# Kernel optimization log

Measured on AMD Instinct MI355X. Metric: run time of the kernel, lower is better.

## Reference

```python
import jax, jax.numpy as jnp
import numpy as np

H = 256   # hidden_dim
NH = 8    # attention heads, embed_dim = 2*H

def _ln(x, g, b, eps=1e-5):
    m = x.mean(-1, keepdims=True)
    v = ((x - m) ** 2).mean(-1, keepdims=True)
    return (x - m) / jnp.sqrt(v + eps) * g + b


def setup_inputs() -> dict:
    key = jax.random.key(0)
    ks = jax.random.split(key, 16)
    B, T, R, P = 32, 2048, 16, 2
    E = 2 * H
    s = 0.02
    n = lambda k, shp: (jax.random.normal(k, shp, jnp.float32) * s)
    z = lambda shp: jnp.zeros(shp, jnp.float32)
    return {
        "encoded_tasks": jax.random.normal(ks[0], (B, T, E), jnp.float32),
        "context": jax.random.normal(ks[1], (B, H), jnp.float32),
        "preference": jax.random.uniform(ks[2], (B, P), dtype=jnp.float32),
        "pref_W": n(ks[3], (P, H)), "pref_b": z((H,)),
        "ln_g": jnp.ones((H,), jnp.float32), "ln_b": z((H,)),
        "Wq": n(ks[4], (E, E)), "bq": z((E,)),
        "Wk": n(ks[5], (E, E)), "bk": z((E,)),
        "Wv": n(ks[6], (E, E)), "bv": z((E,)),
        "Wo": n(ks[7], (E, E)), "bo": z((E,)),
        "W_ih": n(ks[8], (4 * H, 3 * H)), "b_ih": z((4 * H,)),
        "W_hh": n(ks[9], (4 * H, H)), "b_hh": z((4 * H,)),
        "hW1": n(ks[10], (3 * H, H)), "hb1": z((H,)),
        "hW2": n(ks[11], (H, R)), "hb2": z((R,)),
        "num_steps": 32,
    }


def reference(encoded_tasks, context, preference, pref_W, pref_b, ln_g, ln_b,
              Wq, bq, Wk, bk, Wv, bv, Wo, bo,
              W_ih, b_ih, W_hh, b_hh, hW1, hb1, hW2, hb2, num_steps):
    B, T, E = encoded_tasks.shape
    Dh = E // NH
    scale = 1.0 / jnp.sqrt(jnp.float32(Dh))
    # preference encoder: Linear -> ReLU -> LayerNorm
    pref = _ln(jax.nn.relu(preference @ pref_W + pref_b), ln_g, ln_b)  # [B, H]
    # K/V projections of encoded_tasks are step-invariant: compute once
    K = (encoded_tasks @ Wk + bk).reshape(B, T, NH, Dh)
    V = (encoded_tasks @ Wv + bv).reshape(B, T, NH, Dh)
    h0 = context[:, :H]
    c0 = jnp.zeros_like(h0)

    def step(carry, _):
        h, c = carry
        q = jnp.concatenate([h, pref], axis=-1)              # [B, 2H]
        qh = (q @ Wq + bq).reshape(B, NH, Dh) * scale
        scores = jnp.einsum('bhd,bthd->bht', qh, K)
        w = jax.nn.softmax(scores, axis=-1)
        attn = jnp.einsum('bht,bthd->bhd', w, V).reshape(B, E)
        ctx = attn @ Wo + bo                                  # [B, 2H]
        x = jnp.concatenate([h, ctx[:, :H], pref], axis=-1)   # [B, 3H]
        gates = x @ W_ih.T + b_ih + h @ W_hh.T + b_hh         # [B, 4H]
        i, f, g, o = jnp.split(gates, 4, axis=-1)
        c_new = jax.nn.sigmoid(f) * c + jax.nn.sigmoid(i) * jnp.tanh(g)
        h_new = jax.nn.sigmoid(o) * jnp.tanh(c_new)
        dec = jnp.concatenate([h_new, ctx[:, :H], pref], axis=-1)
        logits = jax.nn.relu(dec @ hW1 + hb1) @ hW2 + hb2     # [B, R]
        return (h_new, c_new), logits

    (_, _), logits = jax.lax.scan(step, (h0, c0), None, length=num_steps)
    return jnp.transpose(logits, (1, 0, 2))  # [B, num_steps, R]
```

## Files before the change

kernel.cpp:

```cpp
#include <hip/hip_runtime.h>
#include <hip/hip_bf16.h>


typedef __bf16 bf16;
typedef __attribute__((ext_vector_type(8))) __bf16 bf16x8;
typedef __attribute__((ext_vector_type(4))) __bf16 bf16x4;
typedef __attribute__((ext_vector_type(4))) float f32x4;
typedef __attribute__((ext_vector_type(2))) float f32x2;

#define B_  32
#define T_  2048
#define H_  256
#define S_  32

static __device__ __forceinline__ float sigmoidf_(float x){ return 1.f/(1.f+__expf(-x)); }
static __device__ __forceinline__ float tanhf_(float x){ float e=__expf(2.f*x); return (e-1.f)/(e+1.f); }

__global__ void prep_misc(const float* __restrict__ Wq, const float* __restrict__ Wk,
                          const float* __restrict__ Wv, const float* __restrict__ Wo,
                          const float* __restrict__ Wih, const float* __restrict__ Whh,
                          const float* __restrict__ context,
                          bf16* __restrict__ WkvT, bf16* __restrict__ WqT, bf16* __restrict__ WoT,
                          bf16* __restrict__ WihB, bf16* __restrict__ WhhB,
                          float* __restrict__ h0, float* __restrict__ c0, float* __restrict__ ctxz)
{
  const int total = 524288+262144+131072+786432+262144+8192+8192+262144;
  for (int i = blockIdx.x*blockDim.x + threadIdx.x; i < total; i += gridDim.x*blockDim.x){
    int x = i;
    if (x < 524288){ int n = x>>9, k = x&511;
      WkvT[x] = (bf16)(n<512 ? Wk[k*512+n] : Wv[k*512+(n-512)]); continue; }
    x -= 524288;
    if (x < 262144){ int n = x>>9, k = x&511; WqT[x] = (bf16)Wq[k*512+n]; continue; }
    x -= 262144;
    if (x < 131072){ int h = x>>14, rem = x&16383, j = rem>>6, d = rem&63;
      WoT[x] = (bf16)Wo[(h*64+d)*512 + j]; continue; }
    x -= 131072;
    if (x < 786432){ WihB[x] = (bf16)Wih[x]; continue; }
    x -= 786432;
    if (x < 262144){ WhhB[x] = (bf16)Whh[x]; continue; }
    x -= 262144;
    if (x < 8192){ h0[x] = context[x]; continue; }
    x -= 8192;
    if (x < 8192){ c0[x] = 0.f; continue; }
    x -= 8192;
    ctxz[x] = 0.f;
  }
}

__global__ __launch_bounds__(256) void prep_pref(const float* __restrict__ preference,
                                                 const float* __restrict__ pref_W,
                                                 const float* __restrict__ pref_b,
                                                 const float* __restrict__ ln_g,
                                                 const float* __restrict__ ln_b,
                                                 float* __restrict__ prefb)
{
  __shared__ float red_[4];
  int b = blockIdx.x, j = threadIdx.x;
  float p0 = preference[b*2], p1 = preference[b*2+1];
  float v = fmaxf(p0*pref_W[j] + p1*pref_W[256+j] + pref_b[j], 0.f);
  float s = v;
  #pragma unroll
  for (int o=32;o;o>>=1) s += __shfl_xor(s,o);
  if ((j&63)==0) red_[j>>6] = s;
  __syncthreads();
  float mean = (red_[0]+red_[1]+red_[2]+red_[3]) * (1.f/256.f);
  __syncthreads();
  float d = v - mean;
  float s2 = d*d;
  #pragma unroll
  for (int o=32;o;o>>=1) s2 += __shfl_xor(s2,o);
  if ((j&63)==0) red_[j>>6] = s2;
  __syncthreads();
  float var = (red_[0]+red_[1]+red_[2]+red_[3]) * (1.f/256.f);
  prefb[b*256+j] = d * rsqrtf(var + 1e-5f) * ln_g[j] + ln_b[j];
}

__global__ __launch_bounds__(256) void gemm_kv(const float* __restrict__ X,
                                               const bf16* __restrict__ WkvT,
                                               const float* __restrict__ bk, const float* __restrict__ bv,
                                               unsigned char* __restrict__ Kf8, unsigned char* __restrict__ Vf8)
{
  __shared__ __align__(16) bf16 As[128*40];
  __shared__ __align__(16) bf16 Bs[128*40];
  int blk = blockIdx.x;
  int bm = ((blk>>6)<<3) | (blk&7);
  int bn = (blk>>3)&7;
  int m0 = bm<<7, n0 = bn<<7;
  int tid = threadIdx.x;
  int lane = tid&63, wave = tid>>6;
  int wm = (wave>>1)<<6, wn = (wave&1)<<6;
  int q = lane>>4, li = lane&15;
  int r = tid>>1, half = tid&1;
  const float* Xrow = &X[(size_t)(m0+r)*512 + half*16];
  const bf16*  Brow = &WkvT[(size_t)(n0+r)*512 + half*16];
  f32x4 acc[4][4];
  #pragma unroll
  for (int a=0;a<4;a++)
    #pragma unroll
    for (int b=0;b<4;b++) acc[a][b] = (f32x4){0.f,0.f,0.f,0.f};

  float4 apf[4]; bf16x8 bpf[2];
  #pragma unroll
  for (int i=0;i<4;i++) apf[i] = *(const float4*)(Xrow + i*4);
  bpf[0] = *(const bf16x8*)(Brow);
  bpf[1] = *(const bf16x8*)(Brow + 8);

  for (int k0=0;k0<512;k0+=32){
    __syncthreads();
    #pragma unroll
    for (int i=0;i<4;i++){
      bf16x4 a4; a4[0]=(bf16)apf[i].x; a4[1]=(bf16)apf[i].y; a4[2]=(bf16)apf[i].z; a4[3]=(bf16)apf[i].w;
      *(bf16x4*)&As[r*40 + half*16 + i*4] = a4;
    }
    *(bf16x8*)&Bs[r*40 + half*16]     = bpf[0];
    *(bf16x8*)&Bs[r*40 + half*16 + 8] = bpf[1];
    __syncthreads();
    if (k0+32 < 512){
      #pragma unroll
      for (int i=0;i<4;i++) apf[i] = *(const float4*)(Xrow + k0+32 + i*4);
      bpf[0] = *(const bf16x8*)(Brow + k0+32);
      bpf[1] = *(const bf16x8*)(Brow + k0+40);
    }
    bf16x8 af[4], bfr[4];
    #pragma unroll
    for (int mt=0;mt<4;mt++) af[mt] = *(const bf16x8*)&As[(wm+mt*16+li)*40 + q*8];
    #pragma unroll
    for (int nt=0;nt<4;nt++) bfr[nt] = *(const bf16x8*)&Bs[(wn+nt*16+li)*40 + q*8];
    #pragma unroll
    for (int mt=0;mt<4;mt++)
      #pragma unroll
      for (int nt=0;nt<4;nt++)
        acc[mt][nt] = __builtin_amdgcn_mfma_f32_16x16x32_bf16(bfr[nt], af[mt], acc[mt][nt], 0,0,0);
  }
  #pragma unroll
  for (int mt=0;mt<4;mt++){
    int mm = m0 + wm + mt*16 + li;
    int b = mm>>11, t = mm&2047;
    #pragma unroll
    for (int nt=0;nt<4;nt++){
      int nb = n0 + wn + nt*16 + q*4;
      const float* bias = (nb<512) ? (bk+nb) : (bv+nb-512);
      unsigned char* dst = (nb<512) ? Kf8 : Vf8;
      int nn = nb & 511;
      int h = nn>>6, d0 = nn&63;
      unsigned int p = 0;
      p = __builtin_amdgcn_cvt_pk_fp8_f32(acc[mt][nt][0]+bias[0], acc[mt][nt][1]+bias[1], p, false);
      p = __builtin_amdgcn_cvt_pk_fp8_f32(acc[mt][nt][2]+bias[2], acc[mt][nt][3]+bias[3], p, true);
      *(unsigned int*)&dst[(((size_t)(b*8+h))*T_ + (size_t)t)*64 + d0] = p;
    }
  }
}

__global__ __launch_bounds__(1024) void attn_step(const unsigned char* __restrict__ Kf8,
                                                  const unsigned char* __restrict__ Vf8,
                                                  const bf16* __restrict__ WqT, const bf16* __restrict__ WoT,
                                                  const float* __restrict__ bq, const float* __restrict__ prefb,
                                                  const float* __restrict__ h_prev, float* __restrict__ ctx_s)
{
  __shared__ float q_s[512];
  __shared__ float qh_s[64];
  __shared__ float aw[16][64];
  __shared__ float zw[16];
  __shared__ float attn_s[64];
  int b = blockIdx.x>>3, h = blockIdx.x&7;
  int tid = threadIdx.x;
  if (tid < 512) q_s[tid] = (tid<256) ? h_prev[b*256+tid] : prefb[b*256+(tid-256)];
  __syncthreads();
  {
    int d = tid>>4, p = tid&15;
    const bf16* wr = &WqT[(size_t)(h*64+d)*512 + p*32];
    const float* qq = &q_s[p*32];
    float s = 0.f;
    #pragma unroll
    for (int i=0;i<4;i++){
      bf16x8 w8 = *(const bf16x8*)&wr[i*8];
      #pragma unroll
      for (int j=0;j<8;j++) s += qq[i*8+j]*(float)w8[j];
    }
    s += __shfl_xor(s,1); s += __shfl_xor(s,2); s += __shfl_xor(s,4); s += __shfl_xor(s,8);
    if (p==0) qh_s[d] = (s + bq[h*64+d])*0.125f;
  }
  __syncthreads();
  int lane = tid&63, wave = tid>>6;
  int ro = lane>>2, dq = lane&3;
  float qhf[16];
  #pragma unroll
  for (int j=0;j<16;j++) qhf[j] = qh_s[dq*16+j];
  const unsigned char* Kb = Kf8 + ((size_t)(b*8+h))*T_*64;
  const unsigned char* Vb = Vf8 + ((size_t)(b*8+h))*T_*64;
  float acc[16];
  #pragma unroll
  for (int j=0;j<16;j++) acc[j]=0.f;
  float z = 0.f;
  #pragma unroll
  for (int it=0; it<8; ++it){
    int t = it*256 + wave*16 + ro;
    uint4 k4 = *(const uint4*)&Kb[(size_t)t*64 + dq*16];
    uint4 v4 = *(const uint4*)&Vb[(size_t)t*64 + dq*16];
    float s = 0.f;
    { f32x2 t0, t1;
      t0 = __builtin_amdgcn_cvt_pk_f32_fp8(k4.x,false); t1 = __builtin_amdgcn_cvt_pk_f32_fp8(k4.x,true);
      s += qhf[0]*t0.x + qhf[1]*t0.y + qhf[2]*t1.x + qhf[3]*t1.y;
      t0 = __builtin_amdgcn_cvt_pk_f32_fp8(k4.y,false); t1 = __builtin_amdgcn_cvt_pk_f32_fp8(k4.y,true);
      s += qhf[4]*t0.x + qhf[5]*t0.y + qhf[6]*t1.x + qhf[7]*t1.y;
      t0 = __builtin_amdgcn_cvt_pk_f32_fp8(k4.z,false); t1 = __builtin_amdgcn_cvt_pk_f32_fp8(k4.z,true);
      s += qhf[8]*t0.x + qhf[9]*t0.y + qhf[10]*t1.x + qhf[11]*t1.y;
      t0 = __builtin_amdgcn_cvt_pk_f32_fp8(k4.w,false); t1 = __builtin_amdgcn_cvt_pk_f32_fp8(k4.w,true);
      s += qhf[12]*t0.x + qhf[13]*t0.y + qhf[14]*t1.x + qhf[15]*t1.y;
    }
    s += __shfl_xor(s,1); s += __shfl_xor(s,2);
    float e = __expf(fminf(s, 80.f));
    z += e;
    { f32x2 t0, t1;
      t0 = __builtin_amdgcn_cvt_pk_f32_fp8(v4.x,false); t1 = __builtin_amdgcn_cvt_pk_f32_fp8(v4.x,true);
      acc[0]+=e*t0.x; acc[1]+=e*t0.y; acc[2]+=e*t1.x; acc[3]+=e*t1.y;
      t0 = __builtin_amdgcn_cvt_pk_f32_fp8(v4.y,false); t1 = __builtin_amdgcn_cvt_pk_f32_fp8(v4.y,true);
      acc[4]+=e*t0.x; acc[5]+=e*t0.y; acc[6]+=e*t1.x; acc[7]+=e*t1.y;
      t0 = __builtin_amdgcn_cvt_pk_f32_fp8(v4.z,false); t1 = __builtin_amdgcn_cvt_pk_f32_fp8(v4.z,true);
      acc[8]+=e*t0.x; acc[9]+=e*t0.y; acc[10]+=e*t1.x; acc[11]+=e*t1.y;
      t0 = __builtin_amdgcn_cvt_pk_f32_fp8(v4.w,false); t1 = __builtin_amdgcn_cvt_pk_f32_fp8(v4.w,true);
      acc[12]+=e*t0.x; acc[13]+=e*t0.y; acc[14]+=e*t1.x; acc[15]+=e*t1.y;
    }
  }
  #pragma unroll
  for (int j=0;j<16;j++){
    acc[j] += __shfl_xor(acc[j],4);
    acc[j] += __shfl_xor(acc[j],8);
    acc[j] += __shfl_xor(acc[j],16);
    acc[j] += __shfl_xor(acc[j],32);
  }
  z += __shfl_xor(z,4); z += __shfl_xor(z,8); z += __shfl_xor(z,16); z += __shfl_xor(z,32);
  if (ro==0){
    #pragma unroll
    for (int j=0;j<16;j++) aw[wave][dq*16+j] = acc[j];
    if (dq==0) zw[wave] = z;
  }
  __syncthreads();
  if (tid < 64){
    float Z = 0.f, a = 0.f;
    #pragma unroll
    for (int w=0;w<16;w++){ Z += zw[w]; a += aw[w][tid]; }
    attn_s[tid] = a / Z;
  }
  __syncthreads();
  {
    int j = tid>>2, p4 = tid&3;
    const bf16* wo = &WoT[(((size_t)h*256)+j)*64 + p4*16];
    const float* at = &attn_s[p4*16];
    float cp = 0.f;
    #pragma unroll
    for (int i=0;i<2;i++){
      bf16x8 w8 = *(const bf16x8*)&wo[i*8];
      #pragma unroll
      for (int u=0;u<8;u++) cp += at[i*8+u]*(float)w8[u];
    }
    cp += __shfl_xor(cp,1); cp += __shfl_xor(cp,2);
    if (p4==0) atomicAdd(&ctx_s[b*256+j], cp);
  }
}

__global__ __launch_bounds__(256) void gates_lstm(const float* __restrict__ h_prev, const float* __restrict__ ctx_s,
                                                  const float* __restrict__ prefb, const float* __restrict__ bo,
                                                  const bf16* __restrict__ WihB, const bf16* __restrict__ WhhB,
                                                  const float* __restrict__ b_ih, const float* __restrict__ b_hh,
                                                  const float* __restrict__ c_prev,
                                                  float* __restrict__ c_out, float* __restrict__ h_out)
{
  __shared__ __align__(16) bf16 xs[32*1032];
  __shared__ float gsum[2][32][18];
  int bk = blockIdx.x;
  int tid = threadIdx.x;
  #pragma unroll
  for (int i=0;i<32;i++){
    int u = i*256 + tid;
    int bb = u>>8, kq = u&255;
    int k = kq*4;
    float v0,v1,v2,v3;
    if (k < 256){
      const float* p = &h_prev[bb*256+k];
      v0=p[0];v1=p[1];v2=p[2];v3=p[3];
    } else if (k < 512){
      int j2 = k-256;
      const float* p = &ctx_s[bb*256+j2];
      v0=p[0]+bo[j2]; v1=p[1]+bo[j2+1]; v2=p[2]+bo[j2+2]; v3=p[3]+bo[j2+3];
    } else if (k < 768){
      const float* p = &prefb[bb*256+(k-512)];
      v0=p[0];v1=p[1];v2=p[2];v3=p[3];
    } else {
      const float* p = &h_prev[bb*256+(k-768)];
      v0=p[0];v1=p[1];v2=p[2];v3=p[3];
    }
    bf16x4 w4; w4[0]=(bf16)v0; w4[1]=(bf16)v1; w4[2]=(bf16)v2; w4[3]=(bf16)v3;
    *(bf16x4*)&xs[bb*1032+k] = w4;
  }
  __syncthreads();
  int lane = tid&63, wave = tid>>6;
  int q = lane>>4, li = lane&15;
  int mt = wave&1, kh = wave>>1;
  int n = (li>>2)*256 + bk*4 + (li&3);
  f32x4 acc = (f32x4){0.f,0.f,0.f,0.f};
  #pragma unroll 4
  for (int kk = kh*512; kk < kh*512+512; kk += 32){
    bf16x8 af = *(const bf16x8*)&xs[(mt*16+li)*1032 + kk + q*8];
    int kg = kk + q*8;
    const bf16* wp = (kg<768) ? &WihB[(size_t)n*768 + kg] : &WhhB[(size_t)n*256 + (kg-768)];
    bf16x8 bfrag = *(const bf16x8*)wp;
    acc = __builtin_amdgcn_mfma_f32_16x16x32_bf16(af, bfrag, acc, 0,0,0);
  }
  #pragma unroll
  for (int r=0;r<4;r++) gsum[kh][mt*16 + q*4 + r][li] = acc[r];
  __syncthreads();
  if (tid < 128){
    int b2 = tid>>2, j2 = tid&3;
    float val[4];
    #pragma unroll
    for (int gg=0; gg<4; gg++){
      int ng = gg*256 + bk*4 + j2;
      val[gg] = gsum[0][b2][gg*4+j2] + gsum[1][b2][gg*4+j2] + b_ih[ng] + b_hh[ng];
    }
    int J = bk*4 + j2;
    float cp = c_prev[b2*256+J];
    float cn = sigmoidf_(val[1])*cp + sigmoidf_(val[0])*tanhf_(val[2]);
    float hn = sigmoidf_(val[3])*tanhf_(cn);
    c_out[b2*256+J] = cn;
    h_out[b2*256+J] = hn;
  }
}

__global__ __launch_bounds__(256) void epilogue_k(const float* __restrict__ h_hist, const float* __restrict__ ctx_all,
                                                  const float* __restrict__ bo,
                                                  const float* __restrict__ prefb, const float* __restrict__ hW1,
                                                  const float* __restrict__ hb1, const float* __restrict__ hW2,
                                                  const float* __restrict__ hb2, float* __restrict__ out)
{
  __shared__ float dec[8][768];
  __shared__ float hid[8][260];
  int blk = blockIdx.x;
  int tid = threadIdx.x;
  #pragma unroll
  for (int i=0;i<8;i++){
    int sb = blk*8+i;
    int s = sb>>5, b = sb&31;
    for (int k=tid; k<768; k+=256){
      float v;
      if (k<256)      v = h_hist[((size_t)(s+1)*32 + b)*256 + k];
      else if (k<512) v = ctx_all[((size_t)s*32 + b)*256 + (k-256)] + bo[k-256];
      else            v = prefb[b*256 + (k-512)];
      dec[i][k] = v;
    }
  }
  __syncthreads();
  float a[8];
  #pragma unroll
  for (int i=0;i<8;i++) a[i]=0.f;
  for (int k=0;k<768;k++){
    float w = hW1[(size_t)k*256 + tid];
    #pragma unroll
    for (int i=0;i<8;i++) a[i] += dec[i][k]*w;
  }
  float b1 = hb1[tid];
  #pragma unroll
  for (int i=0;i<8;i++) hid[i][tid] = fmaxf(a[i]+b1, 0.f);
  __syncthreads();
  if (tid < 128){
    int i = tid>>4, r = tid&15;
    float s2 = 0.f;
    for (int j2=0;j2<256;j2++) s2 += hid[i][j2]*hW2[j2*16+r];
    s2 += hb2[r];
    int sb = blk*8+i;
    int st = sb>>5, b = sb&31;
    out[(size_t)b*512 + st*16 + r] = s2;
  }
}

extern "C" void kernel_launch(void* const* d_in, const int* in_sizes, int n_in,
                              void* d_out, int out_size, void* d_ws, size_t ws_size,
                              hipStream_t stream)
{
  const float* X          = (const float*)d_in[0];
  const float* context    = (const float*)d_in[1];
  const float* preference = (const float*)d_in[2];
  const float* pref_W     = (const float*)d_in[3];
  const float* pref_b     = (const float*)d_in[4];
  const float* ln_g       = (const float*)d_in[5];
  const float* ln_b       = (const float*)d_in[6];
  const float* Wq         = (const float*)d_in[7];
  const float* bq         = (const float*)d_in[8];
  const float* Wk         = (const float*)d_in[9];
  const float* bk         = (const float*)d_in[10];
  const float* Wv         = (const float*)d_in[11];
  const float* bv         = (const float*)d_in[12];
  const float* Wo         = (const float*)d_in[13];
  const float* bo         = (const float*)d_in[14];
  const float* W_ih       = (const float*)d_in[15];
  const float* b_ih       = (const float*)d_in[16];
  const float* W_hh       = (const float*)d_in[17];
  const float* b_hh       = (const float*)d_in[18];
  const float* hW1        = (const float*)d_in[19];
  const float* hb1        = (const float*)d_in[20];
  const float* hW2        = (const float*)d_in[21];
  const float* hb2        = (const float*)d_in[22];
  float* out = (float*)d_out;

  char* ws = (char*)d_ws;
  size_t off = 0;
  auto alloc = [&](size_t bytes)->char*{ char* p = ws+off; off += (bytes+255)&~(size_t)255; return p; };
  unsigned char* Kf8 = (unsigned char*)alloc((size_t)B_*8*T_*64);
  unsigned char* Vf8 = (unsigned char*)alloc((size_t)B_*8*T_*64);
  bf16* WkvT    = (bf16*)alloc(1024ull*512*2);
  bf16* WqT     = (bf16*)alloc(512ull*512*2);
  bf16* WoT     = (bf16*)alloc(8ull*256*64*2);
  bf16* WihB    = (bf16*)alloc(1024ull*768*2);
  bf16* WhhB    = (bf16*)alloc(1024ull*256*2);
  float* prefb  = (float*)alloc(8192ull*4);
  float* h_hist = (float*)alloc(33ull*8192*4);
  float* c_hist = (float*)alloc(33ull*8192*4);
  float* ctx_all= (float*)alloc(32ull*8192*4);
  (void)ws_size; (void)in_sizes; (void)n_in; (void)out_size;

  hipLaunchKernelGGL(prep_misc, dim3(512), dim3(256), 0, stream,
                     Wq,Wk,Wv,Wo,W_ih,W_hh,context,
                     WkvT,WqT,WoT,WihB,WhhB, h_hist, c_hist, ctx_all);
  hipLaunchKernelGGL(prep_pref, dim3(32), dim3(256), 0, stream,
                     preference, pref_W, pref_b, ln_g, ln_b, prefb);
  hipLaunchKernelGGL(gemm_kv, dim3(4096), dim3(256), 0, stream, X, WkvT, bk, bv, Kf8, Vf8);
  for (int s=0;s<S_;s++){
    hipLaunchKernelGGL(attn_step, dim3(256), dim3(1024), 0, stream,
                       Kf8, Vf8, WqT, WoT, bq, prefb,
                       h_hist + (size_t)s*8192, ctx_all + (size_t)s*8192);
    hipLaunchKernelGGL(gates_lstm, dim3(64), dim3(256), 0, stream,
                       h_hist + (size_t)s*8192, ctx_all + (size_t)s*8192,
                       prefb, bo, WihB, WhhB, b_ih, b_hh,
                       c_hist + (size_t)s*8192,
                       c_hist + (size_t)(s+1)*8192, h_hist + (size_t)(s+1)*8192);
  }
  hipLaunchKernelGGL(epilogue_k, dim3(128), dim3(256), 0, stream,
                     h_hist, ctx_all, bo, prefb, hW1, hb1, hW2, hb2, out);
}
```

Measured before the change: 1.730 ms.

## Fuse recurrent steps into one cooperative persistent kernel with grid syncs

Replaces the 64 per-step launches of attention and LSTM-gate kernels with a single cooperative kernel that loops over steps and uses grid.sync between phases. Per-head context partials go to a buffer instead of atomics, and each block computes a slice of the LSTM gates in fp32 straight from the original weights. X is also pre-converted to bf16 in the prep kernel so the K/V GEMM loads bf16 directly. The aims are to remove launch overhead and to halve GEMM A-operand traffic. The cost is grid-wide barriers, fp32 gate weight reads every step, and an extra pass over X to convert it.

```diff
diff --git a/kernel.cpp b/kernel.cpp
--- a/kernel.cpp
+++ b/kernel.cpp
@@ -1,5 +1,8 @@
 #include <hip/hip_runtime.h>
 #include <hip/hip_bf16.h>
+#include <hip/hip_cooperative_groups.h>
+
+namespace cg = cooperative_groups;
 
 
 typedef __bf16 bf16;
@@ -16,17 +19,24 @@
 static __device__ __forceinline__ float sigmoidf_(float x){ return 1.f/(1.f+__expf(-x)); }
 static __device__ __forceinline__ float tanhf_(float x){ float e=__expf(2.f*x); return (e-1.f)/(e+1.f); }
 
-__global__ void prep_misc(const float* __restrict__ Wq, const float* __restrict__ Wk,
+#define NX4_ 8388608
+__global__ void prep_misc(const float* __restrict__ X,
+                          const float* __restrict__ Wq, const float* __restrict__ Wk,
                           const float* __restrict__ Wv, const float* __restrict__ Wo,
-                          const float* __restrict__ Wih, const float* __restrict__ Whh,
                           const float* __restrict__ context,
+                          bf16* __restrict__ Xb,
                           bf16* __restrict__ WkvT, bf16* __restrict__ WqT, bf16* __restrict__ WoT,
-                          bf16* __restrict__ WihB, bf16* __restrict__ WhhB,
-                          float* __restrict__ h0, float* __restrict__ c0, float* __restrict__ ctxz)
-{
-  const int total = 524288+262144+131072+786432+262144+8192+8192+262144;
+                          float* __restrict__ h0, float* __restrict__ c0)
+{
+  const int total = NX4_ + 524288+262144+131072+8192+8192;
   for (int i = blockIdx.x*blockDim.x + threadIdx.x; i < total; i += gridDim.x*blockDim.x){
-    int x = i;
+    if (i < NX4_){
+      float4 x4 = *(const float4*)&X[(size_t)i*4];
+      bf16x4 o; o[0]=(bf16)x4.x; o[1]=(bf16)x4.y; o[2]=(bf16)x4.z; o[3]=(bf16)x4.w;
+      *(bf16x4*)&Xb[(size_t)i*4] = o;
+      continue;
+    }
+    int x = i - NX4_;
     if (x < 524288){ int n = x>>9, k = x&511;
       WkvT[x] = (bf16)(n<512 ? Wk[k*512+n] : Wv[k*512+(n-512)]); continue; }
     x -= 524288;
@@ -35,15 +45,9 @@
     if (x < 131072){ int h = x>>14, rem = x&16383, j = rem>>6, d = rem&63;
       WoT[x] = (bf16)Wo[(h*64+d)*512 + j]; continue; }
     x -= 131072;
-    if (x < 786432){ WihB[x] = (bf16)Wih[x]; continue; }
-    x -= 786432;
-    if (x < 262144){ WhhB[x] = (bf16)Whh[x]; continue; }
-    x -= 262144;
     if (x < 8192){ h0[x] = context[x]; continue; }
     x -= 8192;
-    if (x < 8192){ c0[x] = 0.f; continue; }
-    x -= 8192;
-    ctxz[x] = 0.f;
+    c0[x] = 0.f;
   }
 }
 
@@ -75,7 +79,7 @@
   prefb[b*256+j] = d * rsqrtf(var + 1e-5f) * ln_g[j] + ln_b[j];
 }
 
-__global__ __launch_bounds__(256) void gemm_kv(const float* __restrict__ X,
+__global__ __launch_bounds__(256) void gemm_kv(const bf16* __restrict__ Xb,
                                                const bf16* __restrict__ WkvT,
                                                const float* __restrict__ bk, const float* __restrict__ bv,
                                                unsigned char* __restrict__ Kf8, unsigned char* __restrict__ Vf8)
@@ -90,36 +94,32 @@
   int lane = tid&63, wave = tid>>6;
   int wm = (wave>>1)<<6, wn = (wave&1)<<6;
   int q = lane>>4, li = lane&15;
-  int r = tid>>1, half = tid&1;
-  const float* Xrow = &X[(size_t)(m0+r)*512 + half*16];
-  const bf16*  Brow = &WkvT[(size_t)(n0+r)*512 + half*16];
+  int r0 = tid>>2, oct = tid&3;
+  const bf16* A0 = &Xb[(size_t)(m0+r0)*512 + oct*8];
+  const bf16* A1 = A0 + (size_t)64*512;
+  const bf16* B0 = &WkvT[(size_t)(n0+r0)*512 + oct*8];
+  const bf16* B1 = B0 + (size_t)64*512;
   f32x4 acc[4][4];
   #pragma unroll
   for (int a=0;a<4;a++)
     #pragma unroll
     for (int b=0;b<4;b++) acc[a][b] = (f32x4){0.f,0.f,0.f,0.f};
 
-  float4 apf[4]; bf16x8 bpf[2];
-  #pragma unroll
-  for (int i=0;i<4;i++) apf[i] = *(const float4*)(Xrow + i*4);
-  bpf[0] = *(const bf16x8*)(Brow);
-  bpf[1] = *(const bf16x8*)(Brow + 8);
+  bf16x8 apf0 = *(const bf16x8*)A0, apf1 = *(const bf16x8*)A1;
+  bf16x8 bpf0 = *(const bf16x8*)B0, bpf1 = *(const bf16x8*)B1;
 
   for (int k0=0;k0<512;k0+=32){
     __syncthreads();
-    #pragma unroll
-    for (int i=0;i<4;i++){
-      bf16x4 a4; a4[0]=(bf16)apf[i].x; a4[1]=(bf16)apf[i].y; a4[2]=(bf16)apf[i].z; a4[3]=(bf16)apf[i].w;
-      *(bf16x4*)&As[r*40 + half*16 + i*4] = a4;
-    }
-    *(bf16x8*)&Bs[r*40 + half*16]     = bpf[0];
-    *(bf16x8*)&Bs[r*40 + half*16 + 8] = bpf[1];
+    *(bf16x8*)&As[r0*40+oct*8]      = apf0;
+    *(bf16x8*)&As[(r0+64)*40+oct*8] = apf1;
+    *(bf16x8*)&Bs[r0*40+oct*8]      = bpf0;
+    *(bf16x8*)&Bs[(r0+64)*40+oct*8] = bpf1;
     __syncthreads();
     if (k0+32 < 512){
-      #pragma unroll
-      for (int i=0;i<4;i++) apf[i] = *(const float4*)(Xrow + k0+32 + i*4);
-      bpf[0] = *(const bf16x8*)(Brow + k0+32);
-      bpf[1] = *(const bf16x8*)(Brow + k0+40);
+      apf0 = *(const bf16x8*)(A0 + k0+32);
+      apf1 = *(const bf16x8*)(A1 + k0+32);
+      bpf0 = *(const bf16x8*)(B0 + k0+32);
+      bpf1 = *(const bf16x8*)(B1 + k0+32);
     }
     bf16x8 af[4], bfr[4];
     #pragma unroll
@@ -151,184 +151,170 @@
   }
 }
 
-__global__ __launch_bounds__(1024) void attn_step(const unsigned char* __restrict__ Kf8,
-                                                  const unsigned char* __restrict__ Vf8,
-                                                  const bf16* __restrict__ WqT, const bf16* __restrict__ WoT,
-                                                  const float* __restrict__ bq, const float* __restrict__ prefb,
-                                                  const float* __restrict__ h_prev, float* __restrict__ ctx_s)
-{
+__global__ __launch_bounds__(1024, 4) void loop_k(
+    const unsigned char* __restrict__ Kf8, const unsigned char* __restrict__ Vf8,
+    const bf16* __restrict__ WqT, const bf16* __restrict__ WoT,
+    const float* __restrict__ bq, const float* __restrict__ prefb,
+    const float* __restrict__ Wih, const float* __restrict__ Whh,
+    const float* __restrict__ b_ih, const float* __restrict__ b_hh,
+    const float* __restrict__ bo,
+    float* __restrict__ h_hist, float* __restrict__ c_cur,
+    float* __restrict__ ctx_part, float* __restrict__ ctx_hist)
+{
+  cg::grid_group grid = cg::this_grid();
   __shared__ float q_s[512];
   __shared__ float qh_s[64];
   __shared__ float aw[16][64];
   __shared__ float zw[16];
   __shared__ float attn_s[64];
-  int b = blockIdx.x>>3, h = blockIdx.x&7;
-  int tid = threadIdx.x;
-  if (tid < 512) q_s[tid] = (tid<256) ? h_prev[b*256+tid] : prefb[b*256+(tid-256)];
-  __syncthreads();
-  {
-    int d = tid>>4, p = tid&15;
-    const bf16* wr = &WqT[(size_t)(h*64+d)*512 + p*32];
-    const float* qq = &q_s[p*32];
-    float s = 0.f;
-    #pragma unroll
-    for (int i=0;i<4;i++){
-      bf16x8 w8 = *(const bf16x8*)&wr[i*8];
-      #pragma unroll
-      for (int j=0;j<8;j++) s += qq[i*8+j]*(float)w8[j];
-    }
-    s += __shfl_xor(s,1); s += __shfl_xor(s,2); s += __shfl_xor(s,4); s += __shfl_xor(s,8);
-    if (p==0) qh_s[d] = (s + bq[h*64+d])*0.125f;
-  }
-  __syncthreads();
-  int lane = tid&63, wave = tid>>6;
-  int ro = lane>>2, dq = lane&3;
-  float qhf[16];
-  #pragma unroll
-  for (int j=0;j<16;j++) qhf[j] = qh_s[dq*16+j];
+  __shared__ float xh_s[1024];
+  __shared__ float gv_s[128];
+  const int tid = threadIdx.x;
+  const int b = blockIdx.x>>3, sub = blockIdx.x&7;
+  const int h = sub;
+  const int lane = tid&63, wave = tid>>6;
+  const int ro = lane>>2, dq = lane&3;
   const unsigned char* Kb = Kf8 + ((size_t)(b*8+h))*T_*64;
   const unsigned char* Vb = Vf8 + ((size_t)(b*8+h))*T_*64;
-  float acc[16];
-  #pragma unroll
-  for (int j=0;j<16;j++) acc[j]=0.f;
-  float z = 0.f;
-  #pragma unroll
-  for (int it=0; it<8; ++it){
-    int t = it*256 + wave*16 + ro;
-    uint4 k4 = *(const uint4*)&Kb[(size_t)t*64 + dq*16];
-    uint4 v4 = *(const uint4*)&Vb[(size_t)t*64 + dq*16];
-    float s = 0.f;
-    { f32x2 t0, t1;
-      t0 = __builtin_amdgcn_cvt_pk_f32_fp8(k4.x,false); t1 = __builtin_amdgcn_cvt_pk_f32_fp8(k4.x,true);
-      s += qhf[0]*t0.x + qhf[1]*t0.y + qhf[2]*t1.x + qhf[3]*t1.y;
-      t0 = __builtin_amdgcn_cvt_pk_f32_fp8(k4.y,false); t1 = __builtin_amdgcn_cvt_pk_f32_fp8(k4.y,true);
-      s += qhf[4]*t0.x + qhf[5]*t0.y + qhf[6]*t1.x + qhf[7]*t1.y;
-      t0 = __builtin_amdgcn_cvt_pk_f32_fp8(k4.z,false); t1 = __builtin_amdgcn_cvt_pk_f32_fp8(k4.z,true);
-      s += qhf[8]*t0.x + qhf[9]*t0.y + qhf[10]*t1.x + qhf[11]*t1.y;
-      t0 = __builtin_amdgcn_cvt_pk_f32_fp8(k4.w,false); t1 = __builtin_amdgcn_cvt_pk_f32_fp8(k4.w,true);
-      s += qhf[12]*t0.x + qhf[13]*t0.y + qhf[14]*t1.x + qhf[15]*t1.y;
-    }
-    s += __shfl_xor(s,1); s += __shfl_xor(s,2);
-    float e = __expf(fminf(s, 80.f));
-    z += e;
-    { f32x2 t0, t1;
-      t0 = __builtin_amdgcn_cvt_pk_f32_fp8(v4.x,false); t1 = __builtin_amdgcn_cvt_pk_f32_fp8(v4.x,true);
-      acc[0]+=e*t0.x; acc[1]+=e*t0.y; acc[2]+=e*t1.x; acc[3]+=e*t1.y;
-      t0 = __builtin_amdgcn_cvt_pk_f32_fp8(v4.y,false); t1 = __builtin_amdgcn_cvt_pk_f32_fp8(v4.y,true);
-      acc[4]+=e*t0.x; acc[5]+=e*t0.y; acc[6]+=e*t1.x; acc[7]+=e*t1.y;
-      t0 = __builtin_amdgcn_cvt_pk_f32_fp8(v4.z,false); t1 = __builtin_amdgcn_cvt_pk_f32_fp8(v4.z,true);
-      acc[8]+=e*t0.x; acc[9]+=e*t0.y; acc[10]+=e*t1.x; acc[11]+=e*t1.y;
-      t0 = __builtin_amdgcn_cvt_pk_f32_fp8(v4.w,false); t1 = __builtin_amdgcn_cvt_pk_f32_fp8(v4.w,true);
-      acc[12]+=e*t0.x; acc[13]+=e*t0.y; acc[14]+=e*t1.x; acc[15]+=e*t1.y;
-    }
-  }
-  #pragma unroll
-  for (int j=0;j<16;j++){
-    acc[j] += __shfl_xor(acc[j],4);
-    acc[j] += __shfl_xor(acc[j],8);
-    acc[j] += __shfl_xor(acc[j],16);
-    acc[j] += __shfl_xor(acc[j],32);
-  }
-  z += __shfl_xor(z,4); z += __shfl_xor(z,8); z += __shfl_xor(z,16); z += __shfl_xor(z,32);
-  if (ro==0){
-    #pragma unroll
-    for (int j=0;j<16;j++) aw[wave][dq*16+j] = acc[j];
-    if (dq==0) zw[wave] = z;
-  }
-  __syncthreads();
-  if (tid < 64){
-    float Z = 0.f, a = 0.f;
-    #pragma unroll
-    for (int w=0;w<16;w++){ Z += zw[w]; a += aw[w][tid]; }
-    attn_s[tid] = a / Z;
-  }
-  __syncthreads();
-  {
-    int j = tid>>2, p4 = tid&3;
-    const bf16* wo = &WoT[(((size_t)h*256)+j)*64 + p4*16];
-    const float* at = &attn_s[p4*16];
-    float cp = 0.f;
-    #pragma unroll
-    for (int i=0;i<2;i++){
-      bf16x8 w8 = *(const bf16x8*)&wo[i*8];
+
+  for (int s=0; s<S_; ++s){
+    const float* h_cur = h_hist + (size_t)s*8192;
+    if (tid < 512) q_s[tid] = (tid<256) ? h_cur[b*256+tid] : prefb[b*256+(tid-256)];
+    __syncthreads();
+    {
+      int d = tid>>4, p = tid&15;
+      const bf16* wr = &WqT[(size_t)(h*64+d)*512 + p*32];
+      const float* qq = &q_s[p*32];
+      float sd = 0.f;
       #pragma unroll
-      for (int u=0;u<8;u++) cp += at[i*8+u]*(float)w8[u];
-    }
-    cp += __shfl_xor(cp,1); cp += __shfl_xor(cp,2);
-    if (p4==0) atomicAdd(&ctx_s[b*256+j], cp);
-  }
-}
-
-__global__ __launch_bounds__(256) void gates_lstm(const float* __restrict__ h_prev, const float* __restrict__ ctx_s,
-                                                  const float* __restrict__ prefb, const float* __restrict__ bo,
-                                                  const bf16* __restrict__ WihB, const bf16* __restrict__ WhhB,
-                                                  const float* __restrict__ b_ih, const float* __restrict__ b_hh,
-                                                  const float* __restrict__ c_prev,
-                                                  float* __restrict__ c_out, float* __restrict__ h_out)
-{
-  __shared__ __align__(16) bf16 xs[32*1032];
-  __shared__ float gsum[2][32][18];
-  int bk = blockIdx.x;
-  int tid = threadIdx.x;
-  #pragma unroll
-  for (int i=0;i<32;i++){
-    int u = i*256 + tid;
-    int bb = u>>8, kq = u&255;
-    int k = kq*4;
-    float v0,v1,v2,v3;
-    if (k < 256){
-      const float* p = &h_prev[bb*256+k];
-      v0=p[0];v1=p[1];v2=p[2];v3=p[3];
-    } else if (k < 512){
-      int j2 = k-256;
-      const float* p = &ctx_s[bb*256+j2];
-      v0=p[0]+bo[j2]; v1=p[1]+bo[j2+1]; v2=p[2]+bo[j2+2]; v3=p[3]+bo[j2+3];
-    } else if (k < 768){
-      const float* p = &prefb[bb*256+(k-512)];
-      v0=p[0];v1=p[1];v2=p[2];v3=p[3];
-    } else {
-      const float* p = &h_prev[bb*256+(k-768)];
-      v0=p[0];v1=p[1];v2=p[2];v3=p[3];
-    }
-    bf16x4 w4; w4[0]=(bf16)v0; w4[1]=(bf16)v1; w4[2]=(bf16)v2; w4[3]=(bf16)v3;
-    *(bf16x4*)&xs[bb*1032+k] = w4;
-  }
-  __syncthreads();
-  int lane = tid&63, wave = tid>>6;
-  int q = lane>>4, li = lane&15;
-  int mt = wave&1, kh = wave>>1;
-  int n = (li>>2)*256 + bk*4 + (li&3);
-  f32x4 acc = (f32x4){0.f,0.f,0.f,0.f};
-  #pragma unroll 4
-  for (int kk = kh*512; kk < kh*512+512; kk += 32){
-    bf16x8 af = *(const bf16x8*)&xs[(mt*16+li)*1032 + kk + q*8];
-    int kg = kk + q*8;
-    const bf16* wp = (kg<768) ? &WihB[(size_t)n*768 + kg] : &WhhB[(size_t)n*256 + (kg-768)];
-    bf16x8 bfrag = *(const bf16x8*)wp;
-    acc = __builtin_amdgcn_mfma_f32_16x16x32_bf16(af, bfrag, acc, 0,0,0);
-  }
-  #pragma unroll
-  for (int r=0;r<4;r++) gsum[kh][mt*16 + q*4 + r][li] = acc[r];
-  __syncthreads();
-  if (tid < 128){
-    int b2 = tid>>2, j2 = tid&3;
-    float val[4];
-    #pragma unroll
-    for (int gg=0; gg<4; gg++){
-      int ng = gg*256 + bk*4 + j2;
-      val[gg] = gsum[0][b2][gg*4+j2] + gsum[1][b2][gg*4+j2] + b_ih[ng] + b_hh[ng];
-    }
-    int J = bk*4 + j2;
-    float cp = c_prev[b2*256+J];
-    float cn = sigmoidf_(val[1])*cp + sigmoidf_(val[0])*tanhf_(val[2]);
-    float hn = sigmoidf_(val[3])*tanhf_(cn);
-    c_out[b2*256+J] = cn;
-    h_out[b2*256+J] = hn;
-  }
-}
-
-__global__ __launch_bounds__(256) void epilogue_k(const float* __restrict__ h_hist, const float* __restrict__ ctx_all,
-                                                  const float* __restrict__ bo,
+      for (int i=0;i<4;i++){
+        bf16x8 w8 = *(const bf16x8*)&wr[i*8];
+        #pragma unroll
+        for (int j=0;j<8;j++) sd += qq[i*8+j]*(float)w8[j];
+      }
+      sd += __shfl_xor(sd,1); sd += __shfl_xor(sd,2); sd += __shfl_xor(sd,4); sd += __shfl_xor(sd,8);
+      if (p==0) qh_s[d] = (sd + bq[h*64+d])*0.125f;
+    }
+    __syncthreads();
+    float qhf[16];
+    #pragma unroll
+    for (int j=0;j<16;j++) qhf[j] = qh_s[dq*16+j];
+    float acc[16];
+    #pragma unroll
+    for (int j=0;j<16;j++) acc[j]=0.f;
+    float z = 0.f;
+    #pragma unroll
+    for (int it=0; it<8; ++it){
+      int t = it*256 + wave*16 + ro;
+      uint4 k4 = *(const uint4*)&Kb[(size_t)t*64 + dq*16];
+      uint4 v4 = *(const uint4*)&Vb[(size_t)t*64 + dq*16];
+      float sc = 0.f;
+      { f32x2 t0, t1;
+        t0 = __builtin_amdgcn_cvt_pk_f32_fp8(k4.x,false); t1 = __builtin_amdgcn_cvt_pk_f32_fp8(k4.x,true);
+        sc += qhf[0]*t0.x + qhf[1]*t0.y + qhf[2]*t1.x + qhf[3]*t1.y;
+        t0 = __builtin_amdgcn_cvt_pk_f32_fp8(k4.y,false); t1 = __builtin_amdgcn_cvt_pk_f32_fp8(k4.y,true);
+        sc += qhf[4]*t0.x + qhf[5]*t0.y + qhf[6]*t1.x + qhf[7]*t1.y;
+        t0 = __builtin_amdgcn_cvt_pk_f32_fp8(k4.z,false); t1 = __builtin_amdgcn_cvt_pk_f32_fp8(k4.z,true);
+        sc += qhf[8]*t0.x + qhf[9]*t0.y + qhf[10]*t1.x + qhf[11]*t1.y;
+        t0 = __builtin_amdgcn_cvt_pk_f32_fp8(k4.w,false); t1 = __builtin_amdgcn_cvt_pk_f32_fp8(k4.w,true);
+        sc += qhf[12]*t0.x + qhf[13]*t0.y + qhf[14]*t1.x + qhf[15]*t1.y;
+      }
+      sc += __shfl_xor(sc,1); sc += __shfl_xor(sc,2);
+      float e = __expf(fminf(sc, 80.f));
+      z += e;
+      { f32x2 t0, t1;
+        t0 = __builtin_amdgcn_cvt_pk_f32_fp8(v4.x,false); t1 = __builtin_amdgcn_cvt_pk_f32_fp8(v4.x,true);
+        acc[0]+=e*t0.x; acc[1]+=e*t0.y; acc[2]+=e*t1.x; acc[3]+=e*t1.y;
+        t0 = __builtin_amdgcn_cvt_pk_f32_fp8(v4.y,false); t1 = __builtin_amdgcn_cvt_pk_f32_fp8(v4.y,true);
+        acc[4]+=e*t0.x; acc[5]+=e*t0.y; acc[6]+=e*t1.x; acc[7]+=e*t1.y;
+        t0 = __builtin_amdgcn_cvt_pk_f32_fp8(v4.z,false); t1 = __builtin_amdgcn_cvt_pk_f32_fp8(v4.z,true);
+        acc[8]+=e*t0.x; acc[9]+=e*t0.y; acc[10]+=e*t1.x; acc[11]+=e*t1.y;
+        t0 = __builtin_amdgcn_cvt_pk_f32_fp8(v4.w,false); t1 = __builtin_amdgcn_cvt_pk_f32_fp8(v4.w,true);
+        acc[12]+=e*t0.x; acc[13]+=e*t0.y; acc[14]+=e*t1.x; acc[15]+=e*t1.y;
+      }
+    }
+    #pragma unroll
+    for (int j=0;j<16;j++){
+      acc[j] += __shfl_xor(acc[j],4);
+      acc[j] += __shfl_xor(acc[j],8);
+      acc[j] += __shfl_xor(acc[j],16);
+      acc[j] += __shfl_xor(acc[j],32);
+    }
+    z += __shfl_xor(z,4); z += __shfl_xor(z,8); z += __shfl_xor(z,16); z += __shfl_xor(z,32);
+    if (ro==0){
+      #pragma unroll
+      for (int j=0;j<16;j++) aw[wave][dq*16+j] = acc[j];
+      if (dq==0) zw[wave] = z;
+    }
+    __syncthreads();
+    if (tid < 64){
+      float Z = 0.f, a = 0.f;
+      #pragma unroll
+      for (int w=0;w<16;w++){ Z += zw[w]; a += aw[w][tid]; }
+      attn_s[tid] = a / Z;
+    }
+    __syncthreads();
+    {
+      int j = tid>>2, p4 = tid&3;
+      const bf16* wo = &WoT[(((size_t)h*256)+j)*64 + p4*16];
+      const float* at = &attn_s[p4*16];
+      float cp = 0.f;
+      #pragma unroll
+      for (int i=0;i<2;i++){
+        bf16x8 w8 = *(const bf16x8*)&wo[i*8];
+        #pragma unroll
+        for (int u=0;u<8;u++) cp += at[i*8+u]*(float)w8[u];
+      }
+      cp += __shfl_xor(cp,1); cp += __shfl_xor(cp,2);
+      if (p4==0) ctx_part[(size_t)(b*8+h)*256 + j] = cp;
+    }
+    grid.sync();
+    { int k = tid; float xv;
+      if (k < 256) xv = q_s[k];
+      else if (k < 512){
+        int j2 = k-256;
+        float c8 = bo[j2];
+        #pragma unroll
+        for (int h2=0;h2<8;h2++) c8 += ctx_part[(size_t)(b*8+h2)*256 + j2];
+        xv = c8;
+        if (sub==0) ctx_hist[(size_t)s*8192 + b*256 + j2] = c8;
+      }
+      else if (k < 768) xv = q_s[k-256];
+      else xv = q_s[k-768];
+      xh_s[k] = xv;
+    }
+    __syncthreads();
+    { int n4 = tid>>3, p = tid&7;
+      int g = n4>>5, j = sub*32 + (n4&31);
+      int n = g*256 + j;
+      const float* w; const float* x;
+      if (p < 6){ w = &Wih[(size_t)n*768 + p*128]; x = &xh_s[p*128]; }
+      else      { w = &Whh[(size_t)n*256 + (p-6)*128]; x = &xh_s[768 + (p-6)*128]; }
+      float sum = 0.f;
+      #pragma unroll 8
+      for (int i=0;i<32;i++){
+        float4 w4 = *(const float4*)&w[i*4];
+        const float* xx = &x[i*4];
+        sum += w4.x*xx[0] + w4.y*xx[1] + w4.z*xx[2] + w4.w*xx[3];
+      }
+      sum += __shfl_xor(sum,1); sum += __shfl_xor(sum,2); sum += __shfl_xor(sum,4);
+      if (p==0) gv_s[n4] = sum + b_ih[n] + b_hh[n];
+    }
+    __syncthreads();
+    if (tid < 32){
+      int j = sub*32 + tid;
+      float iv = gv_s[tid], fv = gv_s[32+tid], gg = gv_s[64+tid], ov = gv_s[96+tid];
+      float cp = c_cur[b*256+j];
+      float cn = sigmoidf_(fv)*cp + sigmoidf_(iv)*tanhf_(gg);
+      float hn = sigmoidf_(ov)*tanhf_(cn);
+      c_cur[b*256+j] = cn;
+      h_hist[(size_t)(s+1)*8192 + b*256 + j] = hn;
+    }
+    grid.sync();
+  }
+}
+
+__global__ __launch_bounds__(256) void epilogue_k(const float* __restrict__ h_hist, const float* __restrict__ ctx_hist,
                                                   const float* __restrict__ prefb, const float* __restrict__ hW1,
                                                   const float* __restrict__ hb1, const float* __restrict__ hW2,
                                                   const float* __restrict__ hb2, float* __restrict__ out)
@@ -344,7 +330,7 @@
     for (int k=tid; k<768; k+=256){
       float v;
       if (k<256)      v = h_hist[((size_t)(s+1)*32 + b)*256 + k];
-      else if (k<512) v = ctx_all[((size_t)s*32 + b)*256 + (k-256)] + bo[k-256];
+      else if (k<512) v = ctx_hist[((size_t)s*32 + b)*256 + (k-256)];
       else            v = prefb[b*256 + (k-512)];
       dec[i][k] = v;
     }
@@ -405,35 +391,31 @@
   char* ws = (char*)d_ws;
   size_t off = 0;
   auto alloc = [&](size_t bytes)->char*{ char* p = ws+off; off += (bytes+255)&~(size_t)255; return p; };
+  bf16* Xb           = (bf16*)alloc((size_t)B_*T_*512*2);
   unsigned char* Kf8 = (unsigned char*)alloc((size_t)B_*8*T_*64);
   unsigned char* Vf8 = (unsigned char*)alloc((size_t)B_*8*T_*64);
-  bf16* WkvT    = (bf16*)alloc(1024ull*512*2);
-  bf16* WqT     = (bf16*)alloc(512ull*512*2);
-  bf16* WoT     = (bf16*)alloc(8ull*256*64*2);
-  bf16* WihB    = (bf16*)alloc(1024ull*768*2);
-  bf16* WhhB    = (bf16*)alloc(1024ull*256*2);
-  float* prefb  = (float*)alloc(8192ull*4);
-  float* h_hist = (float*)alloc(33ull*8192*4);
-  float* c_hist = (float*)alloc(33ull*8192*4);
-  float* ctx_all= (float*)alloc(32ull*8192*4);
+  bf16* WkvT     = (bf16*)alloc(1024ull*512*2);
+  bf16* WqT      = (bf16*)alloc(512ull*512*2);
+  bf16* WoT      = (bf16*)alloc(8ull*256*64*2);
+  float* prefb   = (float*)alloc(8192ull*4);
+  float* h_hist  = (float*)alloc(33ull*8192*4);
+  float* c_cur   = (float*)alloc(8192ull*4);
+  float* ctx_part= (float*)alloc(256ull*256*4);
+  float* ctx_hist= (float*)alloc(32ull*8192*4);
   (void)ws_size; (void)in_sizes; (void)n_in; (void)out_size;
 
-  hipLaunchKernelGGL(prep_misc, dim3(512), dim3(256), 0, stream,
-                     Wq,Wk,Wv,Wo,W_ih,W_hh,context,
-                     WkvT,WqT,WoT,WihB,WhhB, h_hist, c_hist, ctx_all);
+  hipLaunchKernelGGL(prep_misc, dim3(2048), dim3(256), 0, stream,
+                     X, Wq,Wk,Wv,Wo, context, Xb, WkvT,WqT,WoT, h_hist, c_cur);
   hipLaunchKernelGGL(prep_pref, dim3(32), dim3(256), 0, stream,
                      preference, pref_W, pref_b, ln_g, ln_b, prefb);
-  hipLaunchKernelGGL(gemm_kv, dim3(4096), dim3(256), 0, stream, X, WkvT, bk, bv, Kf8, Vf8);
-  for (int s=0;s<S_;s++){
-    hipLaunchKernelGGL(attn_step, dim3(256), dim3(1024), 0, stream,
-                       Kf8, Vf8, WqT, WoT, bq, prefb,
-                       h_hist + (size_t)s*8192, ctx_all + (size_t)s*8192);
-    hipLaunchKernelGGL(gates_lstm, dim3(64), dim3(256), 0, stream,
-                       h_hist + (size_t)s*8192, ctx_all + (size_t)s*8192,
-                       prefb, bo, WihB, WhhB, b_ih, b_hh,
-                       c_hist + (size_t)s*8192,
-                       c_hist + (size_t)(s+1)*8192, h_hist + (size_t)(s+1)*8192);
+  hipLaunchKernelGGL(gemm_kv, dim3(4096), dim3(256), 0, stream, Xb, WkvT, bk, bv, Kf8, Vf8);
+  {
+    void* args[] = { (void*)&Kf8, (void*)&Vf8, (void*)&WqT, (void*)&WoT,
+                     (void*)&bq, (void*)&prefb, (void*)&W_ih, (void*)&W_hh,
+                     (void*)&b_ih, (void*)&b_hh, (void*)&bo,
+                     (void*)&h_hist, (void*)&c_cur, (void*)&ctx_part, (void*)&ctx_hist };
+    hipLaunchCooperativeKernel((const void*)loop_k, dim3(256), dim3(1024), args, 0, stream);
   }
   hipLaunchKernelGGL(epilogue_k, dim3(128), dim3(256), 0, stream,
-                     h_hist, ctx_all, bo, prefb, hW1, hb1, hW2, hb2, out);
-}
+                     h_hist, ctx_hist, prefb, hW1, hb1, hW2, hb2, out);
+}
```

Result: slower. 5.061 ms (+192.5%).
